# Kernel tuning notes

Measured on AMD Instinct MI355X. Metric: run time of the kernel, lower is better.

The kernel has to match this reference:

```python
import jax, jax.numpy as jnp
import numpy as np

UNITS = 128
LAYERS = 2
RES_LAYERS = 0  # no residual adds


def _lstm(x, W, U, b):
    """Keras-style LSTM, return_sequences=True, zero initial state.
    x: [B, T, D]; W: [D, 4u]; U: [u, 4u]; b: [4u]. Gate order i,f,g,o.
    Dropout is inactive at inference (Keras semantics), so it is omitted.
    """
    B = x.shape[0]
    u = U.shape[0]
    # Precompute input projections for all timesteps (one big GEMM).
    xg = jnp.einsum('btd,dk->btk', x, W) + b  # [B, T, 4u]

    def step(carry, xt):
        h, c = carry
        z = xt + h @ U  # [B, 4u]
        i, f, g, o = jnp.split(z, 4, axis=-1)
        c = jax.nn.sigmoid(f) * c + jax.nn.sigmoid(i) * jnp.tanh(g)
        h = jax.nn.sigmoid(o) * jnp.tanh(c)
        return (h, c), h

    init = (jnp.zeros((B, u), x.dtype), jnp.zeros((B, u), x.dtype))
    _, hs = jax.lax.scan(step, init, jnp.swapaxes(xg, 0, 1))  # [T, B, u]
    return jnp.swapaxes(hs, 0, 1)  # [B, T, u]


def setup_inputs() -> dict:
    key = jax.random.key(0)
    ks = jax.random.split(key, 5)
    B, T, D = 2048, 200, 128
    x = jax.random.normal(ks[0], (B, T, D), dtype=jnp.float32)
    s = 0.08  # small init scale to avoid gate saturation
    Wf = jax.random.normal(ks[1], (LAYERS, D, 4 * UNITS), dtype=jnp.float32) * s
    Uf = jax.random.normal(ks[2], (LAYERS, UNITS, 4 * UNITS), dtype=jnp.float32) * s
    Wb = jax.random.normal(ks[3], (LAYERS, D, 4 * UNITS), dtype=jnp.float32) * s
    Ub = jax.random.normal(ks[4], (LAYERS, UNITS, 4 * UNITS), dtype=jnp.float32) * s
    bf = jnp.ones((LAYERS, 4 * UNITS), dtype=jnp.float32)  # bias_initializer='ones'
    bb = jnp.ones((LAYERS, 4 * UNITS), dtype=jnp.float32)
    return {"x": x, "Wf": Wf, "Uf": Uf, "bf": bf, "Wb": Wb, "Ub": Ub, "bb": bb}


def reference(x, Wf, Uf, bf, Wb, Ub, bb):
    input_fw = x
    input_bw = x
    for i in range(LAYERS):
        output_fw = _lstm(input_fw, Wf[i], Uf[i], bf[i])
        # go_backwards=True then K.reverse == run on time-reversed input, reverse output
        output_bw = _lstm(input_bw[:, ::-1, :], Wb[i], Ub[i], bb[i])[:, ::-1, :]
        if i >= LAYERS - RES_LAYERS:
            output_fw = output_fw + input_fw
            output_bw = output_bw + input_bw
        input_fw = output_fw
        input_bw = output_bw
    # merge_mode == 'ave'
    return (output_fw + output_bw) * 0.5
```

## Files before the change

kernel.cpp:

```cpp
#include <hip/hip_runtime.h>


#define NB   2048
#define NTT  200
#define ND   128
#define NTHR 512

typedef _Float16 f16x8 __attribute__((ext_vector_type(8)));
typedef _Float16 f16x4 __attribute__((ext_vector_type(4)));
typedef float    f32x4 __attribute__((ext_vector_type(4)));

#define BARRIER() asm volatile("s_waitcnt lgkmcnt(0)\n\ts_barrier" ::: "memory")
#define MFMA16(A,B,C) __builtin_amdgcn_mfma_f32_16x16x32_f16((A),(B),(C),0,0,0)

__device__ __forceinline__ float rcp_f(float x){ return __builtin_amdgcn_rcpf(x); }
__device__ __forceinline__ float sigm(float x){ return rcp_f(1.f + __expf(-x)); }
__device__ __forceinline__ float tanh_f(float x){ return 1.f - 2.f*rcp_f(__expf(2.f*x) + 1.f); }

__global__ void __launch_bounds__(256)
repack_w(const float* __restrict__ Wf, const float* __restrict__ Uf,
         const float* __restrict__ Wb, const float* __restrict__ Ub,
         _Float16* __restrict__ pk)
{
  int flat = blockIdx.x*256 + threadIdx.x;
  int j  = flat & 7;
  int lx = (flat >> 3)  & 63;
  int ks = (flat >> 9)  & 3;
  int CT = (flat >> 11) & 31;
  int m  = (flat >> 16) & 3;
  int dr = (flat >> 18) & 1;
  int k  = ks*32 + (lx >> 4)*8 + j;
  int cc = CT*16 + (lx & 15);
  const float* src = dr ? ((m & 1) ? Ub : Wb) : ((m & 1) ? Uf : Wf);
  int layer = m >> 1;
  pk[flat] = (_Float16)src[((size_t)layer*ND + k)*512 + cc];
}

__global__ void __launch_bounds__(512)
repack_b(const float* __restrict__ bf_, const float* __restrict__ bb_,
         float* __restrict__ bp)
{
  for (int k = 0; k < 16; ++k){
    int flat = threadIdx.x + k*512;
    int i     = flat & 3;
    int layer = (flat >> 2) & 1;
    int l     = (flat >> 3) & 63;
    int w     = (flat >> 9) & 7;
    int dr    = (flat >> 12) & 1;
    const float* B = dr ? bb_ : bf_;
    bp[flat] = B[layer*512 + 16*w + (l & 15) + 128*i];
  }
}

__global__ void __launch_bounds__(NTHR, 2)
bilstm_mfma(const float* __restrict__ x,
            const _Float16* __restrict__ pk,
            float* __restrict__ out)
{
  extern __shared__ char smem_raw[];
  _Float16* u1s = (_Float16*)smem_raw;
  _Float16* h0a = u1s + 65536;
  _Float16* h1a = h0a + 4096;
  _Float16* xb  = h1a + 4096;
  _Float16* cls = xb  + 4096;

  const int tid = threadIdx.x;
  const int dir = blockIdx.y;
  const int b0  = blockIdx.x * 16;
  const int w    = tid >> 6;
  const int l    = tid & 63;
  const int kg   = l >> 4;
  const int unit = 16*w + (l & 15);

  const f16x8* PKH = (const f16x8*)pk;
  const float* bp  = (const float*)(pk + 524288) + (size_t)((dir*8 + w)*64 + l)*8;

  {
    const f16x8* u1g = PKH + (size_t)(dir*4 + 3)*32*4*64;
    f16x8* u1w = (f16x8*)u1s;
    for (int idx = tid; idx < 8192; idx += NTHR) u1w[idx] = u1g[idx];
  }

  f16x8 w0r[4][4], u0r[4][4], w1r[4][4];
  #pragma unroll
  for (int i = 0; i < 4; ++i)
    #pragma unroll
    for (int ks = 0; ks < 4; ++ks){
      w0r[i][ks] = PKH[(size_t)(((dir*4 + 0)*32 + (w + 8*i))*4 + ks)*64 + l];
      u0r[i][ks] = PKH[(size_t)(((dir*4 + 1)*32 + (w + 8*i))*4 + ks)*64 + l];
      w1r[i][ks] = PKH[(size_t)(((dir*4 + 2)*32 + (w + 8*i))*4 + ks)*64 + l];
    }
  const f16x8* u1d = (const f16x8*)u1s;

  for (int i = tid; i < 4096; i += NTHR){
    h0a[i] = (_Float16)0.f; h1a[i] = (_Float16)0.f; cls[i] = (_Float16)0.f;
  }

  const int er = tid >> 5;
  const int ej = (tid & 31) * 4;
  const int xidx  = ((ej >> 3) << 7) + (er << 3) + (ej & 7);
  const int hbase = ((unit >> 3) << 7) + (unit & 7);
  const int dstepN = dir ? -ND : ND;

  unsigned xoff  = (unsigned)(((b0 + er)*NTT + (dir ? NTT-2 : 1))*ND + ej);
  const unsigned obase = (unsigned)((b0 + kg*4)*NTT*ND + unit);
  int teN = (dir ? (NTT-1) : 0) * ND;
  _Float16* cl0 = cls + tid*4;

  {
    float4 xv = *(const float4*)(x + (xoff - dstepN));
    f16x4 hx;
    hx[0]=(_Float16)xv.x; hx[1]=(_Float16)xv.y; hx[2]=(_Float16)xv.z; hx[3]=(_Float16)xv.w;
    *(f16x4*)(xb + xidx) = hx;
  }

  __syncthreads();

  #pragma clang loop unroll(disable)
  for (int t = 0; t < NTT; ++t){
    const int rbo = (t & 1) << 11;
    const int wbo = rbo ^ 2048;

    float4 xv = *(const float4*)(x + xoff);
    if (t + 2 < NTT) xoff += dstepN;

    f32x4 a1[4], a0[4];
    #pragma unroll
    for (int i = 0; i < 4; ++i){ a1[i] = (f32x4){0,0,0,0}; a0[i] = (f32x4){0,0,0,0}; }
    #pragma unroll
    for (int ks = 0; ks < 4; ++ks){
      f16x8 ah0 = *(const f16x8*)(h0a + rbo + ks*512 + l*8);
      f16x8 ah1 = *(const f16x8*)(h1a + rbo + ks*512 + l*8);
      #pragma unroll
      for (int i = 0; i < 4; ++i){
        f16x8 u1f = u1d[((w + 8*i)*4 + ks)*64 + l];
        a1[i] = MFMA16(ah0, w1r[i][ks], a1[i]);
        a1[i] = MFMA16(ah1, u1f,        a1[i]);
      }
      f16x8 axf = *(const f16x8*)(xb + rbo + ks*512 + l*8);
      #pragma unroll
      for (int i = 0; i < 4; ++i){
        a0[i] = MFMA16(axf, w0r[i][ks], a0[i]);
        a0[i] = MFMA16(ah0, u0r[i][ks], a0[i]);
      }
    }

    float4 b0v = *(const float4*)(bp);
    float4 b1v = *(const float4*)(bp + 4);

    if (t > 0){
      const int teoN = teN - dstepN;
      f16x4 c1h = *(const f16x4*)(cl0 + 2048);
      f16x4 c1n;
      #pragma unroll
      for (int q = 0; q < 4; ++q){
        float ig = sigm(a1[0][q] + b1v.x);
        float fg = sigm(a1[1][q] + b1v.y);
        float gg = tanh_f(a1[2][q] + b1v.z);
        float og = sigm(a1[3][q] + b1v.w);
        float cv = __builtin_fmaf(fg, (float)c1h[q], ig*gg);
        c1n[q] = (_Float16)cv;
        float hh = og * tanh_f(cv);
        h1a[wbo + hbase + (kg*4 + q)*8] = (_Float16)hh;
        atomicAdd(out + (obase + (unsigned)(q*NTT*ND) + (unsigned)teoN), 0.5f*hh);
      }
      *(f16x4*)(cl0 + 2048) = c1n;
    }

    {
      f16x4 c0h = *(const f16x4*)(cl0);
      f16x4 c0n;
      #pragma unroll
      for (int q = 0; q < 4; ++q){
        float ig = sigm(a0[0][q] + b0v.x);
        float fg = sigm(a0[1][q] + b0v.y);
        float gg = tanh_f(a0[2][q] + b0v.z);
        float og = sigm(a0[3][q] + b0v.w);
        float cv = __builtin_fmaf(fg, (float)c0h[q], ig*gg);
        c0n[q] = (_Float16)cv;
        float hh = og * tanh_f(cv);
        h0a[wbo + hbase + (kg*4 + q)*8] = (_Float16)hh;
      }
      *(f16x4*)(cl0) = c0n;
    }

    {
      f16x4 hx;
      hx[0]=(_Float16)xv.x; hx[1]=(_Float16)xv.y; hx[2]=(_Float16)xv.z; hx[3]=(_Float16)xv.w;
      *(f16x4*)(xb + wbo + xidx) = hx;
    }

    BARRIER();
    teN += dstepN;
  }

  {
    f32x4 a1[4];
    #pragma unroll
    for (int i = 0; i < 4; ++i) a1[i] = (f32x4){0,0,0,0};
    #pragma unroll
    for (int ks = 0; ks < 4; ++ks){
      f16x8 ah0 = *(const f16x8*)(h0a + ks*512 + l*8);
      f16x8 ah1 = *(const f16x8*)(h1a + ks*512 + l*8);
      #pragma unroll
      for (int i = 0; i < 4; ++i){
        f16x8 u1f = u1d[((w + 8*i)*4 + ks)*64 + l];
        a1[i] = MFMA16(ah0, w1r[i][ks], a1[i]);
        a1[i] = MFMA16(ah1, u1f,        a1[i]);
      }
    }
    float4 b1v = *(const float4*)(bp + 4);
    f16x4 c1h = *(const f16x4*)(cl0 + 2048);
    const int teoN = teN - dstepN;
    #pragma unroll
    for (int q = 0; q < 4; ++q){
      float ig = sigm(a1[0][q] + b1v.x);
      float fg = sigm(a1[1][q] + b1v.y);
      float gg = tanh_f(a1[2][q] + b1v.z);
      float og = sigm(a1[3][q] + b1v.w);
      float cv = __builtin_fmaf(fg, (float)c1h[q], ig*gg);
      float hh = og * tanh_f(cv);
      atomicAdd(out + (obase + (unsigned)(q*NTT*ND) + (unsigned)teoN), 0.5f*hh);
    }
  }
}

extern "C" void kernel_launch(void* const* d_in, const int* in_sizes, int n_in,
                              void* d_out, int out_size, void* d_ws, size_t ws_size,
                              hipStream_t stream)
{
  const float* x  = (const float*)d_in[0];
  const float* Wf = (const float*)d_in[1];
  const float* Uf = (const float*)d_in[2];
  const float* bf = (const float*)d_in[3];
  const float* Wb = (const float*)d_in[4];
  const float* Ub = (const float*)d_in[5];
  const float* bb = (const float*)d_in[6];
  float* out = (float*)d_out;

  _Float16* pk = (_Float16*)d_ws;
  float* bp = (float*)(pk + 524288);

  (void)hipFuncSetAttribute((const void*)bilstm_mfma,
                            hipFuncAttributeMaxDynamicSharedMemorySize, 163840);

  repack_w<<<2048, 256, 0, stream>>>(Wf, Uf, Wb, Ub, pk);
  repack_b<<<1, 512, 0, stream>>>(bf, bb, bp);
  hipMemsetAsync(out, 0, (size_t)out_size*sizeof(float), stream);
  dim3 grid(NB/16, 2), blk(NTHR);
  bilstm_mfma<<<grid, blk, 163840, stream>>>(x, pk, out);
}
```

Before: 609.7 us.

## Stagger layer-0 MFMA and layer-1 cell math across wave halves with priority hints

Splits the per-timestep layer-0 MFMA block from the layer-1 MFMA block. Waves 0-3 run the layer-0 MFMAs before the layer-1 cell update, and waves 4-7 run them after it, so matrix-core work and transcendental VALU work from different waves can overlap on the CU. MFMA sections are wrapped in s_setprio raises. The x global load is moved after the first MFMA block. The cost is code duplication and the chance of scheduler or register-pressure side effects, and the staggered orders may simply serialise at the barrier anyway.

```diff
diff --git a/kernel.cpp b/kernel.cpp
--- a/kernel.cpp
+++ b/kernel.cpp
@@ -71,6 +71,7 @@
   const int l    = tid & 63;
   const int kg   = l >> 4;
   const int unit = 16*w + (l & 15);
+  const bool roleA = (w < 4);
 
   const f16x8* PKH = (const f16x8*)pk;
   const float* bp  = (const float*)(pk + 524288) + (size_t)((dir*8 + w)*64 + l)*8;
@@ -121,12 +122,11 @@
     const int rbo = (t & 1) << 11;
     const int wbo = rbo ^ 2048;
 
-    float4 xv = *(const float4*)(x + xoff);
-    if (t + 2 < NTT) xoff += dstepN;
-
     f32x4 a1[4], a0[4];
     #pragma unroll
     for (int i = 0; i < 4; ++i){ a1[i] = (f32x4){0,0,0,0}; a0[i] = (f32x4){0,0,0,0}; }
+
+    __builtin_amdgcn_s_setprio(1);
     #pragma unroll
     for (int ks = 0; ks < 4; ++ks){
       f16x8 ah0 = *(const f16x8*)(h0a + rbo + ks*512 + l*8);
@@ -137,35 +137,58 @@
         a1[i] = MFMA16(ah0, w1r[i][ks], a1[i]);
         a1[i] = MFMA16(ah1, u1f,        a1[i]);
       }
-      f16x8 axf = *(const f16x8*)(xb + rbo + ks*512 + l*8);
-      #pragma unroll
-      for (int i = 0; i < 4; ++i){
-        a0[i] = MFMA16(axf, w0r[i][ks], a0[i]);
-        a0[i] = MFMA16(ah0, u0r[i][ks], a0[i]);
-      }
-    }
-
+    }
+    __builtin_amdgcn_s_setprio(0);
+
+    float4 xv = *(const float4*)(x + xoff);
+    if (t + 2 < NTT) xoff += dstepN;
+    float4 b1v = *(const float4*)(bp + 4);
     float4 b0v = *(const float4*)(bp);
-    float4 b1v = *(const float4*)(bp + 4);
-
-    if (t > 0){
-      const int teoN = teN - dstepN;
-      f16x4 c1h = *(const f16x4*)(cl0 + 2048);
-      f16x4 c1n;
-      #pragma unroll
-      for (int q = 0; q < 4; ++q){
-        float ig = sigm(a1[0][q] + b1v.x);
-        float fg = sigm(a1[1][q] + b1v.y);
-        float gg = tanh_f(a1[2][q] + b1v.z);
-        float og = sigm(a1[3][q] + b1v.w);
-        float cv = __builtin_fmaf(fg, (float)c1h[q], ig*gg);
-        c1n[q] = (_Float16)cv;
-        float hh = og * tanh_f(cv);
-        h1a[wbo + hbase + (kg*4 + q)*8] = (_Float16)hh;
-        atomicAdd(out + (obase + (unsigned)(q*NTT*ND) + (unsigned)teoN), 0.5f*hh);
-      }
-      *(f16x4*)(cl0 + 2048) = c1n;
-    }
+
+#define A0BLOCK()                                                             \
+    { __builtin_amdgcn_s_setprio(1);                                         \
+      _Pragma("unroll")                                                       \
+      for (int ks = 0; ks < 4; ++ks){                                         \
+        f16x8 axf = *(const f16x8*)(xb  + rbo + ks*512 + l*8);                \
+        f16x8 ah0 = *(const f16x8*)(h0a + rbo + ks*512 + l*8);                \
+        _Pragma("unroll")                                                     \
+        for (int i = 0; i < 4; ++i){                                          \
+          a0[i] = MFMA16(axf, w0r[i][ks], a0[i]);                             \
+          a0[i] = MFMA16(ah0, u0r[i][ks], a0[i]);                             \
+        }                                                                     \
+      }                                                                       \
+      __builtin_amdgcn_s_setprio(0);                                         \
+    }
+
+#define CELL1()                                                               \
+    if (t > 0){                                                               \
+      const int teoN = teN - dstepN;                                          \
+      f16x4 c1h = *(const f16x4*)(cl0 + 2048);                                \
+      f16x4 c1n;                                                              \
+      _Pragma("unroll")                                                       \
+      for (int q = 0; q < 4; ++q){                                            \
+        float ig = sigm(a1[0][q] + b1v.x);                                    \
+        float fg = sigm(a1[1][q] + b1v.y);                                    \
+        float gg = tanh_f(a1[2][q] + b1v.z);                                  \
+        float og = sigm(a1[3][q] + b1v.w);                                    \
+        float cv = __builtin_fmaf(fg, (float)c1h[q], ig*gg);                  \
+        c1n[q] = (_Float16)cv;                                                \
+        float hh = og * tanh_f(cv);                                           \
+        h1a[wbo + hbase + (kg*4 + q)*8] = (_Float16)hh;                       \
+        atomicAdd(out + (obase + (unsigned)(q*NTT*ND) + (unsigned)teoN), 0.5f*hh); \
+      }                                                                       \
+      *(f16x4*)(cl0 + 2048) = c1n;                                            \
+    }
+
+    if (roleA){
+      A0BLOCK()
+      CELL1()
+    } else {
+      CELL1()
+      A0BLOCK()
+    }
+#undef A0BLOCK
+#undef CELL1
 
     {
       f16x4 c0h = *(const f16x4*)(cl0);
```

Result: slower. 637.5 us (+4.6%).
